# Optimization experiments

Hardware: AMD Instinct MI355X
Metric: run time of the kernel (lower is better)

Reference implementation:

```python
import jax, jax.numpy as jnp
import numpy as np

VOCAB, ENC, EMB, DEC, ATT = 10000, 2048, 512, 512, 512
B, P, S = 64, 196, 20
PAD_ID = 0


def setup_inputs() -> dict:
    key = jax.random.key(0)
    ks = jax.random.split(key, 20)
    sc = lambda *sh: 1.0 / np.sqrt(sh[-1])
    def lin(k, out, inp):
        kw, kb = jax.random.split(k)
        s = 1.0 / np.sqrt(inp)
        return (jax.random.uniform(kw, (out, inp), jnp.float32, -s, s),
                jax.random.uniform(kb, (out,), jnp.float32, -s, s))
    wenc_w, wenc_b = lin(ks[0], ATT, ENC)
    wdec_w, wdec_b = lin(ks[1], ATT, DEC)
    V_w, V_b = lin(ks[2], 1, ATT)
    h0_w, h0_b = lin(ks[3], DEC, ENC)
    c0_w, c0_b = lin(ks[4], DEC, ENC)
    W_ih, b_ih = lin(ks[5], 4 * DEC, ENC + EMB)
    W_hh, b_hh = lin(ks[6], 4 * DEC, DEC)
    fc_w, fc_b = lin(ks[7], VOCAB, DEC)
    embed_w = jax.random.normal(ks[8], (VOCAB, EMB), jnp.float32)
    embed_w = embed_w.at[PAD_ID].set(0.0)  # padding_idx row is zero
    image_feat = jax.random.normal(ks[9], (B, P, ENC), jnp.float32)
    captions_ids = jax.random.randint(ks[10], (B, S), 0, VOCAB)
    return dict(image_feat=image_feat, captions_ids=captions_ids,
                wenc_w=wenc_w, wenc_b=wenc_b, wdec_w=wdec_w, wdec_b=wdec_b,
                V_w=V_w, V_b=V_b, embed_w=embed_w,
                h0_w=h0_w, h0_b=h0_b, c0_w=c0_w, c0_b=c0_b,
                W_ih=W_ih, b_ih=b_ih, W_hh=W_hh, b_hh=b_hh,
                fc_w=fc_w, fc_b=fc_b)


def reference(image_feat, captions_ids, wenc_w, wenc_b, wdec_w, wdec_b,
              V_w, V_b, embed_w, h0_w, h0_b, c0_w, c0_b,
              W_ih, b_ih, W_hh, b_hh, fc_w, fc_b):
    # eval mode: no input noise, dropout = identity
    avg = image_feat.mean(axis=1)                                   # [B, ENC]
    h = jax.nn.relu(avg @ h0_w.T + h0_b)                            # [B, DEC]
    c = jax.nn.relu(avg @ c0_w.T + c0_b)
    enc_proj = jnp.einsum('bpe,ae->bpa', image_feat, wenc_w) + wenc_b  # [B,P,ATT]
    emb_seq = embed_w[captions_ids]                                 # [B,S,EMB]
    emb_seq = jnp.transpose(emb_seq, (1, 0, 2))                     # [S,B,EMB]

    def step(carry, emb_t):
        h, c = carry
        att = jnp.tanh(enc_proj + (h @ wdec_w.T + wdec_b)[:, None, :])  # [B,P,ATT]
        e = jnp.einsum('bpa,a->bp', att, V_w[0]) + V_b[0]               # [B,P]
        w = jax.nn.softmax(e, axis=1)
        ctx = jnp.einsum('bp,bpe->be', w, image_feat)                   # [B,ENC]
        x = jnp.concatenate([ctx, emb_t], axis=1)                       # [B,ENC+EMB]
        gates = x @ W_ih.T + b_ih + h @ W_hh.T + b_hh                   # [B,4*DEC]
        i, f, g, o = jnp.split(gates, 4, axis=1)
        c_new = jax.nn.sigmoid(f) * c + jax.nn.sigmoid(i) * jnp.tanh(g)
        h_new = jax.nn.sigmoid(o) * jnp.tanh(c_new)
        logits = h_new @ fc_w.T + fc_b                                  # [B,VOCAB]
        return (h_new, c_new), logits

    _, preds = jax.lax.scan(step, (h, c), emb_seq)                  # [S,B,VOCAB]
    return jnp.transpose(preds, (1, 0, 2))                          # [B,S,VOCAB]
```

## Files before the change

kernel.cpp:

```cpp
#include <hip/hip_runtime.h>
#include <hip/hip_bf16.h>

#define DEV static __device__ __forceinline__

typedef short s16x8 __attribute__((ext_vector_type(8)));
typedef float f32x4 __attribute__((ext_vector_type(4)));
typedef unsigned short u16;

constexpr int Bn = 64, Pn = 196, ENCn = 2048, EMBn = 512, DECn = 512, ATTn = 512;
constexpr int VOCABn = 10000, Sn = 20;

DEV u16 f2bf(float x) {
  union { float f; unsigned u; } v; v.f = x;
  unsigned r = v.u + 0x7fffu + ((v.u >> 16) & 1u);
  return (u16)(r >> 16);
}
DEV float bf2f(u16 b) {
  union { unsigned u; float f; } v; v.u = ((unsigned)b) << 16;
  return v.f;
}
DEV float sigm(float x) { return 1.f / (1.f + __expf(-x)); }
DEV float tanh_fast(float x) {
  float e = __expf(2.f * x);
  return 1.f - 2.f / (e + 1.f);
}

DEV s16x8 ld8(const u16* p) { return *reinterpret_cast<const s16x8*>(p); }
DEV f32x4 mfma(s16x8 a, s16x8 b, f32x4 c) {
  return __builtin_amdgcn_mfma_f32_16x16x32_bf16(a, b, c, 0, 0, 0);
}

#define GLOAD_LDS16(gsrc, ldst)                                                \
  __builtin_amdgcn_global_load_lds(                                            \
      (const __attribute__((address_space(1))) void*)(gsrc),                   \
      (__attribute__((address_space(3))) void*)(ldst), 16, 0, 0)

__global__ __launch_bounds__(256) void k_cvtfeat_part(
    const float* __restrict__ feat, u16* __restrict__ featbf,
    float* __restrict__ pavg) {
  int b = blockIdx.y, px = blockIdx.x;
  int d8 = threadIdx.x * 8;
  const float* p = feat + ((size_t)b * Pn + px * 7) * ENCn + d8;
  u16* q = featbf + ((size_t)b * Pn + px * 7) * ENCn + d8;
  float acc[8] = {};
#pragma unroll
  for (int k = 0; k < 7; k++) {
    float4 v0 = *(const float4*)(p + (size_t)k * ENCn);
    float4 v1 = *(const float4*)(p + (size_t)k * ENCn + 4);
    acc[0] += v0.x; acc[1] += v0.y; acc[2] += v0.z; acc[3] += v0.w;
    acc[4] += v1.x; acc[5] += v1.y; acc[6] += v1.z; acc[7] += v1.w;
    s16x8 o;
    o[0] = (short)f2bf(v0.x); o[1] = (short)f2bf(v0.y);
    o[2] = (short)f2bf(v0.z); o[3] = (short)f2bf(v0.w);
    o[4] = (short)f2bf(v1.x); o[5] = (short)f2bf(v1.y);
    o[6] = (short)f2bf(v1.z); o[7] = (short)f2bf(v1.w);
    *(s16x8*)(q + (size_t)k * ENCn) = o;
  }
  float* pp = pavg + ((size_t)px * Bn + b) * ENCn + d8;
  *(f32x4*)pp = f32x4{acc[0], acc[1], acc[2], acc[3]};
  *(f32x4*)(pp + 4) = f32x4{acc[4], acc[5], acc[6], acc[7]};
}

__global__ void k_cvt_all(
    const float* __restrict__ wenc, const float* __restrict__ wdec,
    u16* __restrict__ wdec_bf,
    const float* __restrict__ Wih, u16* __restrict__ Wih_bf,
    const float* __restrict__ Whh, u16* __restrict__ Whh_bf,
    const float* __restrict__ fcw, u16* __restrict__ fcw_bf,
    const float* __restrict__ embw, u16* __restrict__ emb_bf,
    const float* __restrict__ h0w, u16* __restrict__ h0w_bf,
    const float* __restrict__ c0w, u16* __restrict__ c0w_bf,
    u16* __restrict__ Wall, u16* __restrict__ wdecT,
    const float* __restrict__ pavg, u16* __restrict__ avgbf) {
  int gid = blockIdx.x * 256 + threadIdx.x, stride = gridDim.x * 256;
  auto run = [&](const float* __restrict__ s, u16* __restrict__ d, int n8) {
    for (int i = gid; i < n8; i += stride) {
      const float4* sp = (const float4*)(s + (size_t)i * 8);
      float4 a = sp[0], b = sp[1];
      s16x8 o;
      o[0] = (short)f2bf(a.x); o[1] = (short)f2bf(a.y);
      o[2] = (short)f2bf(a.z); o[3] = (short)f2bf(a.w);
      o[4] = (short)f2bf(b.x); o[5] = (short)f2bf(b.y);
      o[6] = (short)f2bf(b.z); o[7] = (short)f2bf(b.w);
      *(s16x8*)(d + (size_t)i * 8) = o;
    }
  };
  run(wdec, wdec_bf, 32768);
  run(Wih, Wih_bf, 655360);
  run(Whh, Whh_bf, 131072);
  run(fcw, fcw_bf, 640000);
  run(embw, emb_bf, 640000);
  run(h0w, h0w_bf, 131072);
  run(c0w, c0w_bf, 131072);
  for (int i = gid; i < 655360; i += stride) {
    int row = i >> 8, k8 = (i & 255) * 8;
    const float* src = (row < 2048)
        ? Wih + (size_t)((row >> 2) + (row & 3) * 512) * 2560 + k8
        : wenc + (size_t)(row - 2048) * 2048 + k8;
    float4 a = *(const float4*)src, b = *(const float4*)(src + 4);
    s16x8 o;
    o[0] = (short)f2bf(a.x); o[1] = (short)f2bf(a.y);
    o[2] = (short)f2bf(a.z); o[3] = (short)f2bf(a.w);
    o[4] = (short)f2bf(b.x); o[5] = (short)f2bf(b.y);
    o[6] = (short)f2bf(b.z); o[7] = (short)f2bf(b.w);
    *(s16x8*)(Wall + (size_t)i * 8) = o;
  }
  for (int i = gid; i < 262144; i += stride) {
    int n = i >> 9, k = i & 511;
    wdecT[(size_t)k * 512 + n] = f2bf(wdec[i]);
  }
  for (int i = gid; i < 16384; i += stride) {
    int b = i >> 8, e8 = (i & 255) * 8;
    float s[8] = {};
#pragma unroll 4
    for (int px = 0; px < 28; px++) {
      const float* pp = pavg + ((size_t)px * Bn + b) * ENCn + e8;
      float4 v0 = *(const float4*)pp, v1 = *(const float4*)(pp + 4);
      s[0] += v0.x; s[1] += v0.y; s[2] += v0.z; s[3] += v0.w;
      s[4] += v1.x; s[5] += v1.y; s[6] += v1.z; s[7] += v1.w;
    }
    s16x8 o;
#pragma unroll
    for (int j = 0; j < 8; j++) o[j] = (short)f2bf(s[j] * (1.f / 196.f));
    *(s16x8*)(avgbf + (size_t)b * ENCn + e8) = o;
  }
}

__global__ __launch_bounds__(256) void k_h0c0(
    const u16* __restrict__ avgbf,
    const u16* __restrict__ h0wbf, const float* __restrict__ h0b,
    const u16* __restrict__ c0wbf, const float* __restrict__ c0b,
    u16* __restrict__ h0out, float* __restrict__ c0out,
    float* __restrict__ decpart) {
  int idx = blockIdx.x * 256 + threadIdx.x;
  float* dz = decpart + (size_t)Bn * 512;
#pragma unroll
  for (int j = 0; j < 6; j++) dz[(size_t)j * 16384 + idx] = 0.f;

  int wid = threadIdx.x >> 6, lane = threadIdx.x & 63;
  int r = lane & 15, hi = lane >> 4;
  bool isC = blockIdx.x >= 32;
  int n0 = ((int)blockIdx.x & 31) * 16;
  const u16* W = (isC ? c0wbf : h0wbf) + (size_t)(n0 + r) * ENCn + hi * 8;
  const u16* ap = avgbf + (size_t)(wid * 16 + r) * ENCn + hi * 8;
  f32x4 acc = {0.f, 0.f, 0.f, 0.f};
#pragma unroll 4
  for (int k = 0; k < ENCn; k += 32) acc = mfma(ld8(ap + k), ld8(W + k), acc);
  int col = n0 + r;
  float bb = (isC ? c0b : h0b)[col];
#pragma unroll
  for (int j = 0; j < 4; j++) {
    int row = wid * 16 + hi * 4 + j;
    float v = fmaxf(acc[j] + bb, 0.f);
    if (isC) c0out[(size_t)row * DECn + col] = v;
    else     h0out[(size_t)row * DECn + col] = f2bf(v);
  }
}

template<typename TA, typename TW, int K>
__global__ __launch_bounds__(256) void k_lin64(
    const TA* __restrict__ A, const TW* __restrict__ W,
    const float* __restrict__ bias1, float* __restrict__ outF, size_t ldo) {
  int wid = threadIdx.x >> 6, lane = threadIdx.x & 63;
  int r = lane & 15, hi = lane >> 4;
  int n0 = blockIdx.x * 16;
  const TA* ap = A + (size_t)(wid * 16 + r) * K + hi * 8;
  const TW* wp = W + (size_t)(n0 + r) * K + hi * 8;
  f32x4 acc = {0.f, 0.f, 0.f, 0.f};
  for (int k = 0; k < K; k += 32) acc = mfma(ld8(ap + k), ld8(wp + k), acc);
  int col = n0 + r;
  float bb = bias1 ? bias1[col] : 0.f;
#pragma unroll
  for (int j = 0; j < 4; j++) {
    int row = wid * 16 + hi * 4 + j;
    outF[(size_t)row * ldo + col] = acc[j] + bb;
  }
}

__global__ __launch_bounds__(256) void k_bigproj(
    const u16* __restrict__ Abf, const u16* __restrict__ Wall,
    const float* __restrict__ encb,
    u16* __restrict__ G, u16* __restrict__ encp) {
  __shared__ u16 As[128][32];
  __shared__ u16 Bs[128][32];
  int tid = threadIdx.x;
  int wid = tid >> 6, lane = tid & 63, r = lane & 15, hi = lane >> 4;
  int wm = wid >> 1, wn = wid & 1;
  int m0 = blockIdx.y * 128, n0 = blockIdx.x * 128;
  int srow = tid >> 2, scol = (tid & 3) * 8;
  const u16* ga  = Abf  + (size_t)(m0 + srow) * ENCn + scol;
  const u16* gb1 = Wall + (size_t)(n0 + srow) * 2048 + scol;
  const u16* gb2 = Wall + (size_t)(n0 + 64 + srow) * 2048 + scol;
  u16* As1 = &As[0][0];
  u16* Bs1 = &Bs[0][0];
  f32x4 acc[4][4] = {};
  for (int k0 = 0; k0 < ENCn; k0 += 32) {
    GLOAD_LDS16(ga + k0,                      As1 + wid * 512);
    GLOAD_LDS16(ga + k0 + (size_t)64 * ENCn,  As1 + 2048 + wid * 512);
    GLOAD_LDS16(gb1 + k0,                     Bs1 + wid * 512);
    GLOAD_LDS16(gb2 + k0,                     Bs1 + 2048 + wid * 512);
    __syncthreads();
    s16x8 af[4], bfr[4];
#pragma unroll
    for (int i = 0; i < 4; i++) af[i]  = *(const s16x8*)(As1 + (wm * 64 + i * 16 + r) * 32 + hi * 8);
#pragma unroll
    for (int j = 0; j < 4; j++) bfr[j] = *(const s16x8*)(Bs1 + (wn * 64 + j * 16 + r) * 32 + hi * 8);
#pragma unroll
    for (int i = 0; i < 4; i++)
#pragma unroll
      for (int j = 0; j < 4; j++)
        acc[i][j] = mfma(af[i], bfr[j], acc[i][j]);
    __syncthreads();
  }
#pragma unroll
  for (int i = 0; i < 4; i++)
#pragma unroll
    for (int j = 0; j < 4; j++) {
      int col = n0 + wn * 64 + j * 16 + r;
#pragma unroll
      for (int q = 0; q < 4; q++) {
        int row = m0 + wm * 64 + i * 16 + hi * 4 + q;
        if (col < 2048) G[(size_t)row * 2048 + col] = f2bf(acc[i][j][q]);
        else encp[(size_t)row * 512 + (col - 2048)] = f2bf(acc[i][j][q] + encb[col - 2048]);
      }
    }
}

__global__ __launch_bounds__(256) void k_eproj(
    const u16* __restrict__ embbf, const int* __restrict__ caps,
    const u16* __restrict__ Wih, float* __restrict__ E) {
  __shared__ u16 As[128][32];
  __shared__ u16 Bs[128][32];
  int tid = threadIdx.x;
  int wid = tid >> 6, lane = tid & 63, r = lane & 15, hi = lane >> 4;
  int wm = wid >> 1, wn = wid & 1;
  int m0 = blockIdx.y * 128, n0 = blockIdx.x * 128;
  int srow = tid >> 2, scol = (tid & 3) * 8;
  int row1 = m0 + srow, row2 = row1 + 64;
  int id1 = caps[(row1 & 63) * Sn + (row1 >> 6)];
  int id2 = caps[(row2 & 63) * Sn + (row2 >> 6)];
  const u16* ga1 = embbf + (size_t)id1 * 512 + scol;
  const u16* ga2 = embbf + (size_t)id2 * 512 + scol;
  const u16* gb1 = Wih + (size_t)(n0 + srow) * 2560 + 2048 + scol;
  const u16* gb2 = Wih + (size_t)(n0 + 64 + srow) * 2560 + 2048 + scol;
  u16* As1 = &As[0][0];
  u16* Bs1 = &Bs[0][0];
  f32x4 acc[4][4] = {};
  for (int k0 = 0; k0 < 512; k0 += 32) {
    GLOAD_LDS16(ga1 + k0, As1 + wid * 512);
    GLOAD_LDS16(ga2 + k0, As1 + 2048 + wid * 512);
    GLOAD_LDS16(gb1 + k0, Bs1 + wid * 512);
    GLOAD_LDS16(gb2 + k0, Bs1 + 2048 + wid * 512);
    __syncthreads();
    s16x8 af[4], bfr[4];
#pragma unroll
    for (int i = 0; i < 4; i++) af[i]  = *(const s16x8*)(As1 + (wm * 64 + i * 16 + r) * 32 + hi * 8);
#pragma unroll
    for (int j = 0; j < 4; j++) bfr[j] = *(const s16x8*)(Bs1 + (wn * 64 + j * 16 + r) * 32 + hi * 8);
#pragma unroll
    for (int i = 0; i < 4; i++)
#pragma unroll
      for (int j = 0; j < 4; j++)
        acc[i][j] = mfma(af[i], bfr[j], acc[i][j]);
    __syncthreads();
  }
#pragma unroll
  for (int i = 0; i < 4; i++)
#pragma unroll
    for (int j = 0; j < 4; j++) {
      int col = n0 + wn * 64 + j * 16 + r;
#pragma unroll
      for (int q = 0; q < 4; q++) {
        int row = m0 + wm * 64 + i * 16 + hi * 4 + q;
        E[(size_t)row * 2048 + col] = acc[i][j][q];
      }
    }
}

__global__ __launch_bounds__(256) void k_step1(
    const u16* __restrict__ encp, const float* __restrict__ decpart,
    const float* __restrict__ wdecb,
    const float* __restrict__ Vw, const float* __restrict__ Vb,
    float* __restrict__ e_s,
    const u16* __restrict__ hin, const u16* __restrict__ Whh,
    float* __restrict__ p2) {
  int bx = blockIdx.x, by = blockIdx.y;
  int wid = threadIdx.x >> 6, lane = threadIdx.x & 63;
  if (bx < 49) {
    int p = bx * 4 + wid, b = by;
    int cb = lane * 8;
    float4 dv0 = *(const float4*)(wdecb + cb);
    float4 dv1 = *(const float4*)(wdecb + cb + 4);
#pragma unroll
    for (int q = 0; q < 4; q++) {
      const float* dq = decpart + ((size_t)q * Bn + b) * 512 + cb;
      float4 v0 = *(const float4*)dq, v1 = *(const float4*)(dq + 4);
      dv0.x += v0.x; dv0.y += v0.y; dv0.z += v0.z; dv0.w += v0.w;
      dv1.x += v1.x; dv1.y += v1.y; dv1.z += v1.z; dv1.w += v1.w;
    }
    float4 vv0 = *(const float4*)(Vw + cb), vv1 = *(const float4*)(Vw + cb + 4);
    s16x8 ev = *(const s16x8*)(encp + (((size_t)(b * Pn + p)) << 9) + cb);
    float s = 0.f;
    s += vv0.x * tanh_fast(bf2f((u16)ev[0]) + dv0.x);
    s += vv0.y * tanh_fast(bf2f((u16)ev[1]) + dv0.y);
    s += vv0.z * tanh_fast(bf2f((u16)ev[2]) + dv0.z);
    s += vv0.w * tanh_fast(bf2f((u16)ev[3]) + dv0.w);
    s += vv1.x * tanh_fast(bf2f((u16)ev[4]) + dv1.x);
    s += vv1.y * tanh_fast(bf2f((u16)ev[5]) + dv1.y);
    s += vv1.z * tanh_fast(bf2f((u16)ev[6]) + dv1.z);
    s += vv1.w * tanh_fast(bf2f((u16)ev[7]) + dv1.w);
    for (int m = 32; m; m >>= 1) s += __shfl_xor(s, m);
    if (lane == 0) e_s[(size_t)b * Pn + p] = s + Vb[0];
  } else {
    int sb = (bx - 49) * 64 + by;
    int n0 = sb * 16;
    int r = lane & 15, hi = lane >> 4;
    int brow = wid * 16 + r;
    f32x4 acc = {0.f, 0.f, 0.f, 0.f};
    const u16* a2 = hin + (size_t)brow * DECn + hi * 8;
    const u16* w2 = Whh + (size_t)(n0 + r) * 512 + hi * 8;
#pragma unroll 4
    for (int k = 0; k < 512; k += 32) acc = mfma(ld8(a2 + k), ld8(w2 + k), acc);
#pragma unroll
    for (int j = 0; j < 4; j++) {
      int row = wid * 16 + hi * 4 + j;
      p2[(size_t)row * 2048 + n0 + r] = acc[j];
    }
  }
}

__global__ __launch_bounds__(512) void k_step2(
    const float* __restrict__ e_s, const u16* __restrict__ G,
    const float* __restrict__ p2, const float* __restrict__ Et,
    const float* __restrict__ bih, const float* __restrict__ bhh,
    float* __restrict__ cbuf, u16* __restrict__ hnew,
    const u16* __restrict__ wdecT, float* __restrict__ decpart) {
  __shared__ float sw[Pn];
  __shared__ float red[512];
  __shared__ float pacc[8 * 512];
  __shared__ float hsh[128];
  int b = blockIdx.y, c = blockIdx.x, tid = threadIdx.x;
  float ev = (tid < Pn) ? e_s[(size_t)b * Pn + tid] : -3.0e38f;
  red[tid] = ev; __syncthreads();
  for (int s = 256; s > 0; s >>= 1) { if (tid < s) red[tid] = fmaxf(red[tid], red[tid + s]); __syncthreads(); }
  float m = red[0]; __syncthreads();
  float ex = (tid < Pn) ? __expf(ev - m) : 0.f;
  red[tid] = ex; __syncthreads();
  for (int s = 256; s > 0; s >>= 1) { if (tid < s) red[tid] += red[tid + s]; __syncthreads(); }
  float inv = 1.f / red[0];
  if (tid < Pn) sw[tid] = ex * inv;
  __syncthreads();
  int g = tid >> 6, t64 = tid & 63;
  int dloc = t64 * 8;
  const u16* gp = G + (size_t)b * Pn * 2048 + c * 512 + dloc;
  float acc[8] = {};
#pragma unroll 2
  for (int p = g; p < Pn; p += 8) {
    float w = sw[p];
    s16x8 v = *(const s16x8*)(gp + (size_t)p * 2048);
#pragma unroll
    for (int j = 0; j < 8; j++) acc[j] += w * bf2f((u16)v[j]);
  }
#pragma unroll
  for (int j = 0; j < 8; j++) pacc[g * 512 + j * 64 + t64] = acc[j];
  __syncthreads();
  if (tid < 128) {
    int d = c * 128 + tid;
    float gv[4];
#pragma unroll
    for (int gg = 0; gg < 4; gg++) {
      int lc = tid * 4 + gg;
      int ia = (lc & 7) * 64 + (lc >> 3);
      float s = 0.f;
#pragma unroll
      for (int gr = 0; gr < 8; gr++) s += pacc[gr * 512 + ia];
      int col = gg * 512 + d;
      gv[gg] = s + p2[(size_t)b * 2048 + col] + Et[(size_t)b * 2048 + col]
             + bih[col] + bhh[col];
    }
    size_t ci = (size_t)b * DECn + d;
    float cn = sigm(gv[1]) * cbuf[ci] + sigm(gv[0]) * tanh_fast(gv[2]);
    float hn = sigm(gv[3]) * tanh_fast(cn);
    cbuf[ci] = cn;
    hnew[ci] = f2bf(hn);
    hsh[tid] = hn;
  }
  __syncthreads();
  float a0 = 0.f;
#pragma unroll 8
  for (int k = 0; k < 128; k++)
    a0 += hsh[k] * bf2f(wdecT[(size_t)(c * 128 + k) * 512 + tid]);
  decpart[((size_t)c * Bn + b) * 512 + tid] = a0;
}

__global__ __launch_bounds__(256) void k_logits(
    const u16* __restrict__ hA, const u16* __restrict__ Wbf,
    const float* __restrict__ bias, float* __restrict__ out) {
  __shared__ u16 As[128][32];
  __shared__ u16 Bs[128][32];
  int tid = threadIdx.x;
  int wid = tid >> 6, lane = tid & 63, r = lane & 15, hi = lane >> 4;
  int wm = wid >> 1, wn = wid & 1;
  int m0 = blockIdx.y * 128, n0 = blockIdx.x * 128;
  int srow = tid >> 2, scol = (tid & 3) * 8;
  const u16* ga = hA + (size_t)(m0 + srow) * 512 + scol;
  int br1 = n0 + srow;       if (br1 > VOCABn - 1) br1 = VOCABn - 1;
  int br2 = n0 + 64 + srow;  if (br2 > VOCABn - 1) br2 = VOCABn - 1;
  const u16* gb1 = Wbf + (size_t)br1 * 512 + scol;
  const u16* gb2 = Wbf + (size_t)br2 * 512 + scol;
  u16* As1 = &As[0][0];
  u16* Bs1 = &Bs[0][0];
  f32x4 acc[4][4] = {};
  for (int k0 = 0; k0 < 512; k0 += 32) {
    GLOAD_LDS16(ga + k0,                     As1 + wid * 512);
    GLOAD_LDS16(ga + k0 + (size_t)64 * 512,  As1 + 2048 + wid * 512);
    GLOAD_LDS16(gb1 + k0,                    Bs1 + wid * 512);
    GLOAD_LDS16(gb2 + k0,                    Bs1 + 2048 + wid * 512);
    __syncthreads();
    s16x8 af[4], bfr[4];
#pragma unroll
    for (int i = 0; i < 4; i++) af[i]  = *(const s16x8*)(As1 + (wm * 64 + i * 16 + r) * 32 + hi * 8);
#pragma unroll
    for (int j = 0; j < 4; j++) bfr[j] = *(const s16x8*)(Bs1 + (wn * 64 + j * 16 + r) * 32 + hi * 8);
#pragma unroll
    for (int i = 0; i < 4; i++)
#pragma unroll
      for (int j = 0; j < 4; j++)
        acc[i][j] = mfma(af[i], bfr[j], acc[i][j]);
    __syncthreads();
  }
#pragma unroll
  for (int i = 0; i < 4; i++)
#pragma unroll
    for (int j = 0; j < 4; j++) {
      int col = n0 + wn * 64 + j * 16 + r;
      if (col < VOCABn) {
        float bb = bias[col];
#pragma unroll
        for (int q = 0; q < 4; q++) {
          int row = m0 + wm * 64 + i * 16 + hi * 4 + q;
          int tt = row >> 6, b = row & 63;
          out[((size_t)b * Sn + tt) * VOCABn + col] = acc[i][j][q] + bb;
        }
      }
    }
}

extern "C" void kernel_launch(void* const* d_in, const int* in_sizes, int n_in,
                              void* d_out, int out_size, void* d_ws, size_t ws_size,
                              hipStream_t stream) {
  const float* image_feat = (const float*)d_in[0];
  const int*   captions   = (const int*)d_in[1];
  const float* wenc_w = (const float*)d_in[2];
  const float* wenc_b = (const float*)d_in[3];
  const float* wdec_w = (const float*)d_in[4];
  const float* wdec_b = (const float*)d_in[5];
  const float* V_w    = (const float*)d_in[6];
  const float* V_b    = (const float*)d_in[7];
  const float* embed_w = (const float*)d_in[8];
  const float* h0_w = (const float*)d_in[9];
  const float* h0_b = (const float*)d_in[10];
  const float* c0_w = (const float*)d_in[11];
  const float* c0_b = (const float*)d_in[12];
  const float* W_ih = (const float*)d_in[13];
  const float* b_ih = (const float*)d_in[14];
  const float* W_hh = (const float*)d_in[15];
  const float* b_hh = (const float*)d_in[16];
  const float* fc_w = (const float*)d_in[17];
  const float* fc_b = (const float*)d_in[18];
  float* out = (float*)d_out;

  char* w = (char*)d_ws;
  auto alloc = [&](size_t bytes) { void* p = (void*)w; w += (bytes + 255) & ~(size_t)255; return p; };
  u16* if_bf   = (u16*)alloc(sizeof(u16) * (size_t)Bn * Pn * ENCn);
  u16* Gbuf    = (u16*)alloc(sizeof(u16) * (size_t)Bn * Pn * 2048);
  u16* Wall    = (u16*)alloc(sizeof(u16) * (size_t)2560 * 2048);
  u16* wdec_bf = (u16*)alloc(sizeof(u16) * (size_t)ATTn * DECn);
  u16* wdecT   = (u16*)alloc(sizeof(u16) * (size_t)DECn * DECn);
  u16* Wih_bf  = (u16*)alloc(sizeof(u16) * (size_t)2048 * 2560);
  u16* Whh_bf  = (u16*)alloc(sizeof(u16) * (size_t)2048 * 512);
  u16* fcw_bf  = (u16*)alloc(sizeof(u16) * (size_t)VOCABn * DECn);
  u16* emb_bf  = (u16*)alloc(sizeof(u16) * (size_t)VOCABn * EMBn);
  u16* h0w_bf  = (u16*)alloc(sizeof(u16) * (size_t)DECn * ENCn);
  u16* c0w_bf  = (u16*)alloc(sizeof(u16) * (size_t)DECn * ENCn);
  u16* avg_bf  = (u16*)alloc(sizeof(u16) * (size_t)Bn * ENCn);
  u16* hall    = (u16*)alloc(sizeof(u16) * (size_t)(Sn + 1) * Bn * DECn);
  u16* encp    = (u16*)alloc(sizeof(u16) * (size_t)Bn * Pn * ATTn);
  float* Ebuf  = (float*)alloc(sizeof(float) * (size_t)Sn * Bn * 2048);
  float* pavg  = (float*)alloc(sizeof(float) * (size_t)28 * Bn * ENCn);
  float* e_s   = (float*)alloc(sizeof(float) * (size_t)Bn * Pn);
  float* cbuf  = (float*)alloc(sizeof(float) * (size_t)Bn * DECn);
  float* p2    = (float*)alloc(sizeof(float) * (size_t)Bn * 2048);
  float* decpart = (float*)alloc(sizeof(float) * (size_t)4 * Bn * 512);

  k_cvtfeat_part<<<dim3(28, Bn), 256, 0, stream>>>(image_feat, if_bf, pavg);
  k_cvt_all<<<2048, 256, 0, stream>>>(wenc_w, wdec_w, wdec_bf,
                                      W_ih, Wih_bf, W_hh, Whh_bf,
                                      fc_w, fcw_bf, embed_w, emb_bf,
                                      h0_w, h0w_bf, c0_w, c0w_bf,
                                      Wall, wdecT, pavg, avg_bf);
  k_bigproj<<<dim3(20, 98), 256, 0, stream>>>(if_bf, Wall, wenc_b, Gbuf, encp);
  k_eproj<<<dim3(16, 10), 256, 0, stream>>>(emb_bf, captions, Wih_bf, Ebuf);
  k_h0c0<<<64, 256, 0, stream>>>(avg_bf, h0w_bf, h0_b, c0w_bf, c0_b,
                                 hall, cbuf, decpart);
  k_lin64<u16, u16, 512><<<32, 256, 0, stream>>>(hall, wdec_bf, nullptr, decpart, 512);

  for (int t = 0; t < Sn; t++) {
    const u16* hin = hall + (size_t)t * Bn * DECn;
    u16* hnew = hall + (size_t)(t + 1) * Bn * DECn;
    k_step1<<<dim3(51, Bn), 256, 0, stream>>>(encp, decpart, wdec_b, V_w, V_b, e_s,
                                              hin, Whh_bf, p2);
    k_step2<<<dim3(4, Bn), 512, 0, stream>>>(e_s, Gbuf, p2,
                                             Ebuf + (size_t)t * Bn * 2048,
                                             b_ih, b_hh, cbuf, hnew, wdecT, decpart);
  }
  k_logits<<<dim3(79, 10), 256, 0, stream>>>(hall + (size_t)Bn * DECn, fcw_bf, fc_b, out);
}
```

Before: 979.2 us.

## Fuse per-step attention scores and recurrent Whh partials into one step kernel

Merges the two per-timestep kernels into a single k_step launch. Each block now recomputes the attention scores for its batch row (redundantly across the 4 column blocks) and computes partial h@W_hh products from a transposed bf16 W_hh, written to ping-pong partial buffers that the next step sums. This halves the launches in the sequential loop and drops the e_s/p2 round trips, at the cost of redundant tanh work, extra partial-sum reads, a new transposed weight copy, and splitting the big projection GEMM into two launches.

```diff
diff --git a/kernel.cpp b/kernel.cpp
--- a/kernel.cpp
+++ b/kernel.cpp
@@ -70,7 +70,7 @@
     const float* __restrict__ embw, u16* __restrict__ emb_bf,
     const float* __restrict__ h0w, u16* __restrict__ h0w_bf,
     const float* __restrict__ c0w, u16* __restrict__ c0w_bf,
-    u16* __restrict__ Wall, u16* __restrict__ wdecT,
+    u16* __restrict__ Wall, u16* __restrict__ wdecT, u16* __restrict__ WhhT,
     const float* __restrict__ pavg, u16* __restrict__ avgbf) {
   int gid = blockIdx.x * 256 + threadIdx.x, stride = gridDim.x * 256;
   auto run = [&](const float* __restrict__ s, u16* __restrict__ d, int n8) {
@@ -109,6 +109,10 @@
     int n = i >> 9, k = i & 511;
     wdecT[(size_t)k * 512 + n] = f2bf(wdec[i]);
   }
+  for (int i = gid; i < 1048576; i += stride) {
+    int k = i >> 11, col = i & 2047;
+    WhhT[i] = f2bf(Whh[(size_t)col * 512 + k]);
+  }
   for (int i = gid; i < 16384; i += stride) {
     int b = i >> 8, e8 = (i & 255) * 8;
     float s[8] = {};
@@ -131,11 +135,14 @@
     const u16* __restrict__ h0wbf, const float* __restrict__ h0b,
     const u16* __restrict__ c0wbf, const float* __restrict__ c0b,
     u16* __restrict__ h0out, float* __restrict__ c0out,
-    float* __restrict__ decpart) {
+    float* __restrict__ decA, float* __restrict__ p2A) {
   int idx = blockIdx.x * 256 + threadIdx.x;
-  float* dz = decpart + (size_t)Bn * 512;
+  float* dz = decA + (size_t)Bn * 512;
 #pragma unroll
   for (int j = 0; j < 6; j++) dz[(size_t)j * 16384 + idx] = 0.f;
+  float* pz = p2A + (size_t)Bn * 2048;
+#pragma unroll
+  for (int j = 0; j < 24; j++) pz[(size_t)j * 16384 + idx] = 0.f;
 
   int wid = threadIdx.x >> 6, lane = threadIdx.x & 63;
   int r = lane & 15, hi = lane >> 4;
@@ -177,10 +184,9 @@
   }
 }
 
-__global__ __launch_bounds__(256) void k_bigproj(
+__global__ __launch_bounds__(256) void k_gproj(
     const u16* __restrict__ Abf, const u16* __restrict__ Wall,
-    const float* __restrict__ encb,
-    u16* __restrict__ G, u16* __restrict__ encp) {
+    u16* __restrict__ G) {
   __shared__ u16 As[128][32];
   __shared__ u16 Bs[128][32];
   int tid = threadIdx.x;
@@ -220,8 +226,55 @@
 #pragma unroll
       for (int q = 0; q < 4; q++) {
         int row = m0 + wm * 64 + i * 16 + hi * 4 + q;
-        if (col < 2048) G[(size_t)row * 2048 + col] = f2bf(acc[i][j][q]);
-        else encp[(size_t)row * 512 + (col - 2048)] = f2bf(acc[i][j][q] + encb[col - 2048]);
+        G[(size_t)row * 2048 + col] = f2bf(acc[i][j][q]);
+      }
+    }
+}
+
+__global__ __launch_bounds__(256) void k_encproj(
+    const u16* __restrict__ Abf, const u16* __restrict__ Wall,
+    const float* __restrict__ encb, u16* __restrict__ encp) {
+  __shared__ u16 As[128][32];
+  __shared__ u16 Bs[128][32];
+  int tid = threadIdx.x;
+  int wid = tid >> 6, lane = tid & 63, r = lane & 15, hi = lane >> 4;
+  int wm = wid >> 1, wn = wid & 1;
+  int m0 = blockIdx.y * 128, n0 = blockIdx.x * 128;
+  int srow = tid >> 2, scol = (tid & 3) * 8;
+  const u16* ga  = Abf  + (size_t)(m0 + srow) * ENCn + scol;
+  const u16* gb1 = Wall + (size_t)(2048 + n0 + srow) * 2048 + scol;
+  const u16* gb2 = Wall + (size_t)(2048 + n0 + 64 + srow) * 2048 + scol;
+  u16* As1 = &As[0][0];
+  u16* Bs1 = &Bs[0][0];
+  f32x4 acc[4][4] = {};
+  for (int k0 = 0; k0 < ENCn; k0 += 32) {
+    GLOAD_LDS16(ga + k0,                      As1 + wid * 512);
+    GLOAD_LDS16(ga + k0 + (size_t)64 * ENCn,  As1 + 2048 + wid * 512);
+    GLOAD_LDS16(gb1 + k0,                     Bs1 + wid * 512);
+    GLOAD_LDS16(gb2 + k0,                     Bs1 + 2048 + wid * 512);
+    __syncthreads();
+    s16x8 af[4], bfr[4];
+#pragma unroll
+    for (int i = 0; i < 4; i++) af[i]  = *(const s16x8*)(As1 + (wm * 64 + i * 16 + r) * 32 + hi * 8);
+#pragma unroll
+    for (int j = 0; j < 4; j++) bfr[j] = *(const s16x8*)(Bs1 + (wn * 64 + j * 16 + r) * 32 + hi * 8);
+#pragma unroll
+    for (int i = 0; i < 4; i++)
+#pragma unroll
+      for (int j = 0; j < 4; j++)
+        acc[i][j] = mfma(af[i], bfr[j], acc[i][j]);
+    __syncthreads();
+  }
+#pragma unroll
+  for (int i = 0; i < 4; i++)
+#pragma unroll
+    for (int j = 0; j < 4; j++) {
+      int col = n0 + wn * 64 + j * 16 + r;
+      float bb = encb[col];
+#pragma unroll
+      for (int q = 0; q < 4; q++) {
+        int row = m0 + wm * 64 + i * 16 + hi * 4 + q;
+        encp[(size_t)row * 512 + col] = f2bf(acc[i][j][q] + bb);
       }
     }
 }
@@ -277,70 +330,52 @@
     }
 }
 
-__global__ __launch_bounds__(256) void k_step1(
-    const u16* __restrict__ encp, const float* __restrict__ decpart,
+__global__ __launch_bounds__(512) void k_step(
+    const u16* __restrict__ encp,
+    const float* __restrict__ decR, float* __restrict__ decW,
+    const float* __restrict__ p2R, float* __restrict__ p2W,
     const float* __restrict__ wdecb,
     const float* __restrict__ Vw, const float* __restrict__ Vb,
-    float* __restrict__ e_s,
-    const u16* __restrict__ hin, const u16* __restrict__ Whh,
-    float* __restrict__ p2) {
-  int bx = blockIdx.x, by = blockIdx.y;
-  int wid = threadIdx.x >> 6, lane = threadIdx.x & 63;
-  if (bx < 49) {
-    int p = bx * 4 + wid, b = by;
-    int cb = lane * 8;
-    float4 dv0 = *(const float4*)(wdecb + cb);
-    float4 dv1 = *(const float4*)(wdecb + cb + 4);
-#pragma unroll
-    for (int q = 0; q < 4; q++) {
-      const float* dq = decpart + ((size_t)q * Bn + b) * 512 + cb;
-      float4 v0 = *(const float4*)dq, v1 = *(const float4*)(dq + 4);
-      dv0.x += v0.x; dv0.y += v0.y; dv0.z += v0.z; dv0.w += v0.w;
-      dv1.x += v1.x; dv1.y += v1.y; dv1.z += v1.z; dv1.w += v1.w;
-    }
-    float4 vv0 = *(const float4*)(Vw + cb), vv1 = *(const float4*)(Vw + cb + 4);
-    s16x8 ev = *(const s16x8*)(encp + (((size_t)(b * Pn + p)) << 9) + cb);
-    float s = 0.f;
-    s += vv0.x * tanh_fast(bf2f((u16)ev[0]) + dv0.x);
-    s += vv0.y * tanh_fast(bf2f((u16)ev[1]) + dv0.y);
-    s += vv0.z * tanh_fast(bf2f((u16)ev[2]) + dv0.z);
-    s += vv0.w * tanh_fast(bf2f((u16)ev[3]) + dv0.w);
-    s += vv1.x * tanh_fast(bf2f((u16)ev[4]) + dv1.x);
-    s += vv1.y * tanh_fast(bf2f((u16)ev[5]) + dv1.y);
-    s += vv1.z * tanh_fast(bf2f((u16)ev[6]) + dv1.z);
-    s += vv1.w * tanh_fast(bf2f((u16)ev[7]) + dv1.w);
-    for (int m = 32; m; m >>= 1) s += __shfl_xor(s, m);
-    if (lane == 0) e_s[(size_t)b * Pn + p] = s + Vb[0];
-  } else {
-    int sb = (bx - 49) * 64 + by;
-    int n0 = sb * 16;
-    int r = lane & 15, hi = lane >> 4;
-    int brow = wid * 16 + r;
-    f32x4 acc = {0.f, 0.f, 0.f, 0.f};
-    const u16* a2 = hin + (size_t)brow * DECn + hi * 8;
-    const u16* w2 = Whh + (size_t)(n0 + r) * 512 + hi * 8;
-#pragma unroll 4
-    for (int k = 0; k < 512; k += 32) acc = mfma(ld8(a2 + k), ld8(w2 + k), acc);
-#pragma unroll
-    for (int j = 0; j < 4; j++) {
-      int row = wid * 16 + hi * 4 + j;
-      p2[(size_t)row * 2048 + n0 + r] = acc[j];
-    }
-  }
-}
-
-__global__ __launch_bounds__(512) void k_step2(
-    const float* __restrict__ e_s, const u16* __restrict__ G,
-    const float* __restrict__ p2, const float* __restrict__ Et,
+    const u16* __restrict__ G, const float* __restrict__ Et,
     const float* __restrict__ bih, const float* __restrict__ bhh,
     float* __restrict__ cbuf, u16* __restrict__ hnew,
-    const u16* __restrict__ wdecT, float* __restrict__ decpart) {
-  __shared__ float sw[Pn];
+    const u16* __restrict__ wdecT, const u16* __restrict__ WhhT) {
+  __shared__ float e_lds[Pn];
   __shared__ float red[512];
   __shared__ float pacc[8 * 512];
   __shared__ float hsh[128];
   int b = blockIdx.y, c = blockIdx.x, tid = threadIdx.x;
-  float ev = (tid < Pn) ? e_s[(size_t)b * Pn + tid] : -3.0e38f;
+  int wv = tid >> 6, lane = tid & 63;
+  {
+    int cb = lane * 8;
+    float4 dv0 = *(const float4*)(wdecb + cb);
+    float4 dv1 = *(const float4*)(wdecb + cb + 4);
+#pragma unroll
+    for (int q = 0; q < 4; q++) {
+      const float* dq = decR + ((size_t)q * Bn + b) * 512 + cb;
+      float4 v0 = *(const float4*)dq, v1 = *(const float4*)(dq + 4);
+      dv0.x += v0.x; dv0.y += v0.y; dv0.z += v0.z; dv0.w += v0.w;
+      dv1.x += v1.x; dv1.y += v1.y; dv1.z += v1.z; dv1.w += v1.w;
+    }
+    float4 vv0 = *(const float4*)(Vw + cb), vv1 = *(const float4*)(Vw + cb + 4);
+    float vb0 = Vb[0];
+    for (int p = wv; p < Pn; p += 8) {
+      s16x8 ev = *(const s16x8*)(encp + (((size_t)(b * Pn + p)) << 9) + cb);
+      float s = 0.f;
+      s += vv0.x * tanh_fast(bf2f((u16)ev[0]) + dv0.x);
+      s += vv0.y * tanh_fast(bf2f((u16)ev[1]) + dv0.y);
+      s += vv0.z * tanh_fast(bf2f((u16)ev[2]) + dv0.z);
+      s += vv0.w * tanh_fast(bf2f((u16)ev[3]) + dv0.w);
+      s += vv1.x * tanh_fast(bf2f((u16)ev[4]) + dv1.x);
+      s += vv1.y * tanh_fast(bf2f((u16)ev[5]) + dv1.y);
+      s += vv1.z * tanh_fast(bf2f((u16)ev[6]) + dv1.z);
+      s += vv1.w * tanh_fast(bf2f((u16)ev[7]) + dv1.w);
+      for (int m = 32; m; m >>= 1) s += __shfl_xor(s, m);
+      if (lane == 0) e_lds[p] = s + vb0;
+    }
+  }
+  __syncthreads();
+  float ev = (tid < Pn) ? e_lds[tid] : -3.0e38f;
   red[tid] = ev; __syncthreads();
   for (int s = 256; s > 0; s >>= 1) { if (tid < s) red[tid] = fmaxf(red[tid], red[tid + s]); __syncthreads(); }
   float m = red[0]; __syncthreads();
@@ -348,15 +383,15 @@
   red[tid] = ex; __syncthreads();
   for (int s = 256; s > 0; s >>= 1) { if (tid < s) red[tid] += red[tid + s]; __syncthreads(); }
   float inv = 1.f / red[0];
-  if (tid < Pn) sw[tid] = ex * inv;
+  if (tid < Pn) e_lds[tid] = ex * inv;
   __syncthreads();
-  int g = tid >> 6, t64 = tid & 63;
+  int g = wv, t64 = lane;
   int dloc = t64 * 8;
   const u16* gp = G + (size_t)b * Pn * 2048 + c * 512 + dloc;
   float acc[8] = {};
 #pragma unroll 2
   for (int p = g; p < Pn; p += 8) {
-    float w = sw[p];
+    float w = e_lds[p];
     s16x8 v = *(const s16x8*)(gp + (size_t)p * 2048);
 #pragma unroll
     for (int j = 0; j < 8; j++) acc[j] += w * bf2f((u16)v[j]);
@@ -375,8 +410,11 @@
 #pragma unroll
       for (int gr = 0; gr < 8; gr++) s += pacc[gr * 512 + ia];
       int col = gg * 512 + d;
-      gv[gg] = s + p2[(size_t)b * 2048 + col] + Et[(size_t)b * 2048 + col]
-             + bih[col] + bhh[col];
+      s += p2R[((size_t)0 * Bn + b) * 2048 + col]
+         + p2R[((size_t)1 * Bn + b) * 2048 + col]
+         + p2R[((size_t)2 * Bn + b) * 2048 + col]
+         + p2R[((size_t)3 * Bn + b) * 2048 + col];
+      gv[gg] = s + Et[(size_t)b * 2048 + col] + bih[col] + bhh[col];
     }
     size_t ci = (size_t)b * DECn + d;
     float cn = sigm(gv[1]) * cbuf[ci] + sigm(gv[0]) * tanh_fast(gv[2]);
@@ -386,11 +424,26 @@
     hsh[tid] = hn;
   }
   __syncthreads();
-  float a0 = 0.f;
+  {
+    float a0 = 0.f;
 #pragma unroll 8
-  for (int k = 0; k < 128; k++)
-    a0 += hsh[k] * bf2f(wdecT[(size_t)(c * 128 + k) * 512 + tid]);
-  decpart[((size_t)c * Bn + b) * 512 + tid] = a0;
+    for (int k = 0; k < 128; k++)
+      a0 += hsh[k] * bf2f(wdecT[(size_t)(c * 128 + k) * 512 + tid]);
+    decW[((size_t)c * Bn + b) * 512 + tid] = a0;
+  }
+  {
+    float b0 = 0.f, b1 = 0.f, b2 = 0.f, b3 = 0.f;
+    int c4 = tid * 4;
+#pragma unroll 8
+    for (int k = 0; k < 128; k++) {
+      float h = hsh[k];
+      const u16* wr = WhhT + (size_t)(c * 128 + k) * 2048 + c4;
+      ushort4 wv4 = *(const ushort4*)wr;
+      b0 += h * bf2f(wv4.x); b1 += h * bf2f(wv4.y);
+      b2 += h * bf2f(wv4.z); b3 += h * bf2f(wv4.w);
+    }
+    *(float4*)(p2W + ((size_t)c * Bn + b) * 2048 + c4) = float4{b0, b1, b2, b3};
+  }
 }
 
 __global__ __launch_bounds__(256) void k_logits(
@@ -477,6 +530,7 @@
   u16* Wall    = (u16*)alloc(sizeof(u16) * (size_t)2560 * 2048);
   u16* wdec_bf = (u16*)alloc(sizeof(u16) * (size_t)ATTn * DECn);
   u16* wdecT   = (u16*)alloc(sizeof(u16) * (size_t)DECn * DECn);
+  u16* WhhT    = (u16*)alloc(sizeof(u16) * (size_t)512 * 2048);
   u16* Wih_bf  = (u16*)alloc(sizeof(u16) * (size_t)2048 * 2560);
   u16* Whh_bf  = (u16*)alloc(sizeof(u16) * (size_t)2048 * 512);
   u16* fcw_bf  = (u16*)alloc(sizeof(u16) * (size_t)VOCABn * DECn);
@@ -488,31 +542,35 @@
   u16* encp    = (u16*)alloc(sizeof(u16) * (size_t)Bn * Pn * ATTn);
   float* Ebuf  = (float*)alloc(sizeof(float) * (size_t)Sn * Bn * 2048);
   float* pavg  = (float*)alloc(sizeof(float) * (size_t)28 * Bn * ENCn);
-  float* e_s   = (float*)alloc(sizeof(float) * (size_t)Bn * Pn);
   float* cbuf  = (float*)alloc(sizeof(float) * (size_t)Bn * DECn);
-  float* p2    = (float*)alloc(sizeof(float) * (size_t)Bn * 2048);
-  float* decpart = (float*)alloc(sizeof(float) * (size_t)4 * Bn * 512);
+  float* decA  = (float*)alloc(sizeof(float) * (size_t)4 * Bn * 512);
+  float* decB  = (float*)alloc(sizeof(float) * (size_t)4 * Bn * 512);
+  float* p2A   = (float*)alloc(sizeof(float) * (size_t)4 * Bn * 2048);
+  float* p2B   = (float*)alloc(sizeof(float) * (size_t)4 * Bn * 2048);
 
   k_cvtfeat_part<<<dim3(28, Bn), 256, 0, stream>>>(image_feat, if_bf, pavg);
   k_cvt_all<<<2048, 256, 0, stream>>>(wenc_w, wdec_w, wdec_bf,
                                       W_ih, Wih_bf, W_hh, Whh_bf,
                                       fc_w, fcw_bf, embed_w, emb_bf,
                                       h0_w, h0w_bf, c0_w, c0w_bf,
-                                      Wall, wdecT, pavg, avg_bf);
-  k_bigproj<<<dim3(20, 98), 256, 0, stream>>>(if_bf, Wall, wenc_b, Gbuf, encp);
+                                      Wall, wdecT, WhhT, pavg, avg_bf);
+  k_gproj<<<dim3(16, 98), 256, 0, stream>>>(if_bf, Wall, Gbuf);
+  k_encproj<<<dim3(4, 98), 256, 0, stream>>>(if_bf, Wall, wenc_b, encp);
   k_eproj<<<dim3(16, 10), 256, 0, stream>>>(emb_bf, captions, Wih_bf, Ebuf);
   k_h0c0<<<64, 256, 0, stream>>>(avg_bf, h0w_bf, h0_b, c0w_bf, c0_b,
-                                 hall, cbuf, decpart);
-  k_lin64<u16, u16, 512><<<32, 256, 0, stream>>>(hall, wdec_bf, nullptr, decpart, 512);
+                                 hall, cbuf, decA, p2A);
+  k_lin64<u16, u16, 512><<<32, 256, 0, stream>>>(hall, wdec_bf, nullptr, decA, 512);
+  k_lin64<u16, u16, 512><<<128, 256, 0, stream>>>(hall, Whh_bf, nullptr, p2A, 2048);
 
   for (int t = 0; t < Sn; t++) {
-    const u16* hin = hall + (size_t)t * Bn * DECn;
     u16* hnew = hall + (size_t)(t + 1) * Bn * DECn;
-    k_step1<<<dim3(51, Bn), 256, 0, stream>>>(encp, decpart, wdec_b, V_w, V_b, e_s,
-                                              hin, Whh_bf, p2);
-    k_step2<<<dim3(4, Bn), 512, 0, stream>>>(e_s, Gbuf, p2,
-                                             Ebuf + (size_t)t * Bn * 2048,
-                                             b_ih, b_hh, cbuf, hnew, wdecT, decpart);
+    const float* dR = (t & 1) ? decB : decA;  float* dW = (t & 1) ? decA : decB;
+    const float* pR = (t & 1) ? p2B : p2A;    float* pW = (t & 1) ? p2A : p2B;
+    k_step<<<dim3(4, Bn), 512, 0, stream>>>(encp, dR, dW, pR, pW,
+                                            wdec_b, V_w, V_b, Gbuf,
+                                            Ebuf + (size_t)t * Bn * 2048,
+                                            b_ih, b_hh, cbuf, hnew,
+                                            wdecT, WhhT);
   }
   k_logits<<<dim3(79, 10), 256, 0, stream>>>(hall + (size_t)Bn * DECn, fcw_bf, fc_b, out);
 }
```

After: 1.199 ms. +22.4%, slower.

## Merge gate and encoder projections into one buffer and remap tiles across XCDs

Applied to the files above, without the earlier changes.

Writes the G and encoder-projection outputs into a single interleaved buffer of row width 2560, so the big projection epilogue takes no branch and no bias. The encoder bias moves into step1, where it is added to the decoder bias. The bigproj and logits grids are flattened, and block ids are remapped so that blocks sharing tiles land on the same XCD and reuse its L2. Only the embedding slice of W_ih is converted instead of the full matrix, which cuts conversion traffic. The trade-off is strided per-step reads through the wider row pitch.

```diff
diff --git a/kernel.cpp b/kernel.cpp
--- a/kernel.cpp
+++ b/kernel.cpp
@@ -9,6 +9,7 @@
 
 constexpr int Bn = 64, Pn = 196, ENCn = 2048, EMBn = 512, DECn = 512, ATTn = 512;
 constexpr int VOCABn = 10000, Sn = 20;
+constexpr int GEW = 2560;
 
 DEV u16 f2bf(float x) {
   union { float f; unsigned u; } v; v.f = x;
@@ -64,7 +65,7 @@
 __global__ void k_cvt_all(
     const float* __restrict__ wenc, const float* __restrict__ wdec,
     u16* __restrict__ wdec_bf,
-    const float* __restrict__ Wih, u16* __restrict__ Wih_bf,
+    const float* __restrict__ Wih, u16* __restrict__ Wemb,
     const float* __restrict__ Whh, u16* __restrict__ Whh_bf,
     const float* __restrict__ fcw, u16* __restrict__ fcw_bf,
     const float* __restrict__ embw, u16* __restrict__ emb_bf,
@@ -86,12 +87,22 @@
     }
   };
   run(wdec, wdec_bf, 32768);
-  run(Wih, Wih_bf, 655360);
   run(Whh, Whh_bf, 131072);
   run(fcw, fcw_bf, 640000);
   run(embw, emb_bf, 640000);
   run(h0w, h0w_bf, 131072);
   run(c0w, c0w_bf, 131072);
+  for (int i = gid; i < 131072; i += stride) {
+    int n = i >> 6, k8 = (i & 63) * 8;
+    const float* src = Wih + (size_t)n * 2560 + 2048 + k8;
+    float4 a = *(const float4*)src, b = *(const float4*)(src + 4);
+    s16x8 o;
+    o[0] = (short)f2bf(a.x); o[1] = (short)f2bf(a.y);
+    o[2] = (short)f2bf(a.z); o[3] = (short)f2bf(a.w);
+    o[4] = (short)f2bf(b.x); o[5] = (short)f2bf(b.y);
+    o[6] = (short)f2bf(b.z); o[7] = (short)f2bf(b.w);
+    *(s16x8*)(Wemb + (size_t)i * 8) = o;
+  }
   for (int i = gid; i < 655360; i += stride) {
     int row = i >> 8, k8 = (i & 255) * 8;
     const float* src = (row < 2048)
@@ -177,16 +188,18 @@
   }
 }
 
-__global__ __launch_bounds__(256) void k_bigproj(
+__global__ __launch_bounds__(256) void k_geproj(
     const u16* __restrict__ Abf, const u16* __restrict__ Wall,
-    const float* __restrict__ encb,
-    u16* __restrict__ G, u16* __restrict__ encp) {
+    u16* __restrict__ GE) {
   __shared__ u16 As[128][32];
   __shared__ u16 Bs[128][32];
+  int lid = blockIdx.x;
+  int w = (lid & 7) * 245 + (lid >> 3);
+  int bx = w % 20, by = w / 20;
   int tid = threadIdx.x;
   int wid = tid >> 6, lane = tid & 63, r = lane & 15, hi = lane >> 4;
   int wm = wid >> 1, wn = wid & 1;
-  int m0 = blockIdx.y * 128, n0 = blockIdx.x * 128;
+  int m0 = by * 128, n0 = bx * 128;
   int srow = tid >> 2, scol = (tid & 3) * 8;
   const u16* ga  = Abf  + (size_t)(m0 + srow) * ENCn + scol;
   const u16* gb1 = Wall + (size_t)(n0 + srow) * 2048 + scol;
@@ -220,15 +233,14 @@
 #pragma unroll
       for (int q = 0; q < 4; q++) {
         int row = m0 + wm * 64 + i * 16 + hi * 4 + q;
-        if (col < 2048) G[(size_t)row * 2048 + col] = f2bf(acc[i][j][q]);
-        else encp[(size_t)row * 512 + (col - 2048)] = f2bf(acc[i][j][q] + encb[col - 2048]);
+        GE[(size_t)row * GEW + col] = f2bf(acc[i][j][q]);
       }
     }
 }
 
 __global__ __launch_bounds__(256) void k_eproj(
     const u16* __restrict__ embbf, const int* __restrict__ caps,
-    const u16* __restrict__ Wih, float* __restrict__ E) {
+    const u16* __restrict__ Wemb, float* __restrict__ E) {
   __shared__ u16 As[128][32];
   __shared__ u16 Bs[128][32];
   int tid = threadIdx.x;
@@ -241,8 +253,8 @@
   int id2 = caps[(row2 & 63) * Sn + (row2 >> 6)];
   const u16* ga1 = embbf + (size_t)id1 * 512 + scol;
   const u16* ga2 = embbf + (size_t)id2 * 512 + scol;
-  const u16* gb1 = Wih + (size_t)(n0 + srow) * 2560 + 2048 + scol;
-  const u16* gb2 = Wih + (size_t)(n0 + 64 + srow) * 2560 + 2048 + scol;
+  const u16* gb1 = Wemb + (size_t)(n0 + srow) * 512 + scol;
+  const u16* gb2 = Wemb + (size_t)(n0 + 64 + srow) * 512 + scol;
   u16* As1 = &As[0][0];
   u16* Bs1 = &Bs[0][0];
   f32x4 acc[4][4] = {};
@@ -278,8 +290,8 @@
 }
 
 __global__ __launch_bounds__(256) void k_step1(
-    const u16* __restrict__ encp, const float* __restrict__ decpart,
-    const float* __restrict__ wdecb,
+    const u16* __restrict__ GE, const float* __restrict__ decpart,
+    const float* __restrict__ wdecb, const float* __restrict__ encb,
     const float* __restrict__ Vw, const float* __restrict__ Vb,
     float* __restrict__ e_s,
     const u16* __restrict__ hin, const u16* __restrict__ Whh,
@@ -289,8 +301,12 @@
   if (bx < 49) {
     int p = bx * 4 + wid, b = by;
     int cb = lane * 8;
+    float4 eb0 = *(const float4*)(encb + cb);
+    float4 eb1 = *(const float4*)(encb + cb + 4);
     float4 dv0 = *(const float4*)(wdecb + cb);
     float4 dv1 = *(const float4*)(wdecb + cb + 4);
+    dv0.x += eb0.x; dv0.y += eb0.y; dv0.z += eb0.z; dv0.w += eb0.w;
+    dv1.x += eb1.x; dv1.y += eb1.y; dv1.z += eb1.z; dv1.w += eb1.w;
 #pragma unroll
     for (int q = 0; q < 4; q++) {
       const float* dq = decpart + ((size_t)q * Bn + b) * 512 + cb;
@@ -299,7 +315,7 @@
       dv1.x += v1.x; dv1.y += v1.y; dv1.z += v1.z; dv1.w += v1.w;
     }
     float4 vv0 = *(const float4*)(Vw + cb), vv1 = *(const float4*)(Vw + cb + 4);
-    s16x8 ev = *(const s16x8*)(encp + (((size_t)(b * Pn + p)) << 9) + cb);
+    s16x8 ev = *(const s16x8*)(GE + (size_t)(b * Pn + p) * GEW + 2048 + cb);
     float s = 0.f;
     s += vv0.x * tanh_fast(bf2f((u16)ev[0]) + dv0.x);
     s += vv0.y * tanh_fast(bf2f((u16)ev[1]) + dv0.y);
@@ -330,7 +346,7 @@
 }
 
 __global__ __launch_bounds__(512) void k_step2(
-    const float* __restrict__ e_s, const u16* __restrict__ G,
+    const float* __restrict__ e_s, const u16* __restrict__ GE,
     const float* __restrict__ p2, const float* __restrict__ Et,
     const float* __restrict__ bih, const float* __restrict__ bhh,
     float* __restrict__ cbuf, u16* __restrict__ hnew,
@@ -352,12 +368,12 @@
   __syncthreads();
   int g = tid >> 6, t64 = tid & 63;
   int dloc = t64 * 8;
-  const u16* gp = G + (size_t)b * Pn * 2048 + c * 512 + dloc;
+  const u16* gp = GE + (size_t)(b * Pn) * GEW + c * 512 + dloc;
   float acc[8] = {};
 #pragma unroll 2
   for (int p = g; p < Pn; p += 8) {
     float w = sw[p];
-    s16x8 v = *(const s16x8*)(gp + (size_t)p * 2048);
+    s16x8 v = *(const s16x8*)(gp + (size_t)p * GEW);
 #pragma unroll
     for (int j = 0; j < 8; j++) acc[j] += w * bf2f((u16)v[j]);
   }
@@ -398,10 +414,14 @@
     const float* __restrict__ bias, float* __restrict__ out) {
   __shared__ u16 As[128][32];
   __shared__ u16 Bs[128][32];
+  int lid = blockIdx.x;
+  int xcd = lid & 7, idx = lid >> 3;
+  int w = (xcd < 6) ? xcd * 99 + idx : 6 * 99 + (xcd - 6) * 98 + idx;
+  int bx = w / 10, by = w % 10;
   int tid = threadIdx.x;
   int wid = tid >> 6, lane = tid & 63, r = lane & 15, hi = lane >> 4;
   int wm = wid >> 1, wn = wid & 1;
-  int m0 = blockIdx.y * 128, n0 = blockIdx.x * 128;
+  int m0 = by * 128, n0 = bx * 128;
   int srow = tid >> 2, scol = (tid & 3) * 8;
   const u16* ga = hA + (size_t)(m0 + srow) * 512 + scol;
   int br1 = n0 + srow;       if (br1 > VOCABn - 1) br1 = VOCABn - 1;
@@ -473,11 +493,11 @@
   char* w = (char*)d_ws;
   auto alloc = [&](size_t bytes) { void* p = (void*)w; w += (bytes + 255) & ~(size_t)255; return p; };
   u16* if_bf   = (u16*)alloc(sizeof(u16) * (size_t)Bn * Pn * ENCn);
-  u16* Gbuf    = (u16*)alloc(sizeof(u16) * (size_t)Bn * Pn * 2048);
+  u16* GEbuf   = (u16*)alloc(sizeof(u16) * (size_t)Bn * Pn * GEW);
   u16* Wall    = (u16*)alloc(sizeof(u16) * (size_t)2560 * 2048);
   u16* wdec_bf = (u16*)alloc(sizeof(u16) * (size_t)ATTn * DECn);
   u16* wdecT   = (u16*)alloc(sizeof(u16) * (size_t)DECn * DECn);
-  u16* Wih_bf  = (u16*)alloc(sizeof(u16) * (size_t)2048 * 2560);
+  u16* Wemb    = (u16*)alloc(sizeof(u16) * (size_t)2048 * 512);
   u16* Whh_bf  = (u16*)alloc(sizeof(u16) * (size_t)2048 * 512);
   u16* fcw_bf  = (u16*)alloc(sizeof(u16) * (size_t)VOCABn * DECn);
   u16* emb_bf  = (u16*)alloc(sizeof(u16) * (size_t)VOCABn * EMBn);
@@ -485,7 +505,6 @@
   u16* c0w_bf  = (u16*)alloc(sizeof(u16) * (size_t)DECn * ENCn);
   u16* avg_bf  = (u16*)alloc(sizeof(u16) * (size_t)Bn * ENCn);
   u16* hall    = (u16*)alloc(sizeof(u16) * (size_t)(Sn + 1) * Bn * DECn);
-  u16* encp    = (u16*)alloc(sizeof(u16) * (size_t)Bn * Pn * ATTn);
   float* Ebuf  = (float*)alloc(sizeof(float) * (size_t)Sn * Bn * 2048);
   float* pavg  = (float*)alloc(sizeof(float) * (size_t)28 * Bn * ENCn);
   float* e_s   = (float*)alloc(sizeof(float) * (size_t)Bn * Pn);
@@ -495,12 +514,12 @@
 
   k_cvtfeat_part<<<dim3(28, Bn), 256, 0, stream>>>(image_feat, if_bf, pavg);
   k_cvt_all<<<2048, 256, 0, stream>>>(wenc_w, wdec_w, wdec_bf,
-                                      W_ih, Wih_bf, W_hh, Whh_bf,
+                                      W_ih, Wemb, W_hh, Whh_bf,
                                       fc_w, fcw_bf, embed_w, emb_bf,
                                       h0_w, h0w_bf, c0_w, c0w_bf,
                                       Wall, wdecT, pavg, avg_bf);
-  k_bigproj<<<dim3(20, 98), 256, 0, stream>>>(if_bf, Wall, wenc_b, Gbuf, encp);
-  k_eproj<<<dim3(16, 10), 256, 0, stream>>>(emb_bf, captions, Wih_bf, Ebuf);
+  k_geproj<<<1960, 256, 0, stream>>>(if_bf, Wall, GEbuf);
+  k_eproj<<<dim3(16, 10), 256, 0, stream>>>(emb_bf, captions, Wemb, Ebuf);
   k_h0c0<<<64, 256, 0, stream>>>(avg_bf, h0w_bf, h0_b, c0w_bf, c0_b,
                                  hall, cbuf, decpart);
   k_lin64<u16, u16, 512><<<32, 256, 0, stream>>>(hall, wdec_bf, nullptr, decpart, 512);
@@ -508,11 +527,11 @@
   for (int t = 0; t < Sn; t++) {
     const u16* hin = hall + (size_t)t * Bn * DECn;
     u16* hnew = hall + (size_t)(t + 1) * Bn * DECn;
-    k_step1<<<dim3(51, Bn), 256, 0, stream>>>(encp, decpart, wdec_b, V_w, V_b, e_s,
-                                              hin, Whh_bf, p2);
-    k_step2<<<dim3(4, Bn), 512, 0, stream>>>(e_s, Gbuf, p2,
+    k_step1<<<dim3(51, Bn), 256, 0, stream>>>(GEbuf, decpart, wdec_b, wenc_b,
+                                              V_w, V_b, e_s, hin, Whh_bf, p2);
+    k_step2<<<dim3(4, Bn), 512, 0, stream>>>(e_s, GEbuf, p2,
                                              Ebuf + (size_t)t * Bn * 2048,
                                              b_ih, b_hh, cbuf, hnew, wdecT, decpart);
   }
-  k_logits<<<dim3(79, 10), 256, 0, stream>>>(hall + (size_t)Bn * DECn, fcw_bf, fc_b, out);
-}
+  k_logits<<<790, 256, 0, stream>>>(hall + (size_t)Bn * DECn, fcw_bf, fc_b, out);
+}
```

New measurement: 944.7 us. 3.5% less time.
